# Kernel optimization log

Measured on AMD Instinct MI355X. Metric: run time of the kernel, lower is better.

## Reference

```python
import jax, jax.numpy as jnp
import numpy as np

T = 4.0  # distillation temperature (init kwarg)
B, C = 64, 1000


def _hierarchical_softmax(x, targets):
    # x, targets: [B, C]
    xd = jax.lax.stop_gradient(x)
    # t2[b,i,k] = relu(x[b,i] - stop_grad(x[b,k]))  -> [B, C, C]
    t2 = jnp.maximum(x[:, :, None] - xd[:, None, :], 0.0)
    # t3[b,i] = mean_k targets[b,k] * t2[b,i,k]
    t3 = (targets[:, None, :] * t2).mean(axis=-1)  # [B, C]
    choice = targets * jnp.exp(-t3) + (1.0 - targets)
    ex = jnp.exp(x)
    neg_sum = ((1.0 - targets) * ex).sum(axis=-1, keepdims=True)  # [B, 1]
    return ex / (choice * neg_sum + ex)


def setup_inputs() -> dict:
    key = jax.random.key(0)
    k1, k2, k3 = jax.random.split(key, 3)
    y_s = jax.random.normal(k1, (B, C), dtype=jnp.float32)
    y_t = jax.random.normal(k2, (B, C), dtype=jnp.float32)
    w = jax.random.randint(k3, (B, C), 0, 2).astype(jnp.float32)  # multi-hot targets
    return {"y_s": y_s, "y_t": y_t, "w": w}


def reference(y_s, y_t, w):
    # 'w' branch of DistillKL.forward (dead code: preds/thr/sigmoid/max_min omitted)
    p_s = _hierarchical_softmax(y_s / 4.0, w)
    p_t = _hierarchical_softmax(y_t / 4.0, w)
    p_s_1 = jnp.minimum(p_s, 1.0)  # clamp(max=1)
    p_t_1 = jnp.minimum(p_t, 1.0)
    # abs(...) >= 0 so clamp(min=0,max=1) == min(.,1)
    pos_expo = w * jnp.minimum(jnp.abs((p_t_1 + 1.0) / 2.0 - p_s_1), 1.0) ** 0.25
    neg_expo = (1.0 - w) * jnp.minimum(jnp.abs(p_t_1 / 2.0 - p_s_1), 1.0)
    expt = pos_expo + neg_expo
    ps = jnp.maximum(p_s_1 ** expt, 1e-7)
    pt = jnp.maximum(p_t, 1e-7)
    # my_kl: -(target * log(pred)).sum(dim=1).mean() * T**2
    return -(pt * jnp.log(ps)).sum(axis=1).mean() * (T * T)
```

## Files before the change

kernel.cpp:

```cpp
#include <hip/hip_runtime.h>


#define BN 64
#define CN 1000
#define CPAD 1024
#define SPLITS 8
#define CHUNK 125
#define THREADS 512
#define KQ (CPAD / 4)
#define NEG_LOG_EPS -16.118095650958319f

__global__ __launch_bounds__(THREADS) void distill_part(
    const float* __restrict__ ys, const float* __restrict__ yt,
    const float* __restrict__ w, float* __restrict__ part)
{
    const int b = blockIdx.x;
    const int s = blockIdx.y;
    const int tid = threadIdx.x;
    const int lane = tid & 63;
    const int wid = tid >> 6;
    const int l = tid & 127;
    const int q = tid >> 7;

    __shared__ __align__(16) float xs[CPAD], xt[CPAD];
    __shared__ __align__(16) float xsm[CPAD], xtm[CPAD];
    __shared__ float wsh[CPAD];
    __shared__ float ps_s[THREADS], ps_t[THREADS];
    __shared__ float redns[16];
    __shared__ float redterm[2];

    const float* ysr = ys + b * CN;
    const float* ytr = yt + b * CN;
    const float* wr  = w  + b * CN;

    float ns_s = 0.f, ns_t = 0.f;
    #pragma unroll
    for (int k = tid; k < CPAD; k += THREADS) {
        if (k < CN) {
            float a  = ysr[k] * 0.25f;
            float c2 = ytr[k] * 0.25f;
            float wk = wr[k];
            xs[k] = a; xt[k] = c2; wsh[k] = wk;
            bool pos = (wk != 0.f);
            xsm[k] = pos ? a  : 1e30f;
            xtm[k] = pos ? c2 : 1e30f;
            float nw = 1.f - wk;
            ns_s += nw * expf(a);
            ns_t += nw * expf(c2);
        } else {
            xs[k] = 0.f; xt[k] = 0.f; wsh[k] = 0.f;
            xsm[k] = 1e30f; xtm[k] = 1e30f;
        }
    }
    #pragma unroll
    for (int off = 32; off > 0; off >>= 1) {
        ns_s += __shfl_down(ns_s, off);
        ns_t += __shfl_down(ns_t, off);
    }
    if (lane == 0) { redns[wid * 2] = ns_s; redns[wid * 2 + 1] = ns_t; }
    __syncthreads();
    float negsum_s = 0.f, negsum_t = 0.f;
    #pragma unroll
    for (int u = 0; u < 8; ++u) {
        negsum_s += redns[u * 2];
        negsum_t += redns[u * 2 + 1];
    }

    const int i = s * CHUNK + l;
    const float xsi = xs[i], xti = xt[i];
    const float4* xsm4 = reinterpret_cast<const float4*>(xsm) + q * (KQ / 4);
    const float4* xtm4 = reinterpret_cast<const float4*>(xtm) + q * (KQ / 4);
    float as0 = 0.f, as1 = 0.f, at0 = 0.f, at1 = 0.f;
    #pragma unroll 4
    for (int j = 0; j < KQ / 4; ++j) {
        float4 vs = xsm4[j];
        float4 vt = xtm4[j];
        as0 += fmaxf(xsi - vs.x, 0.f);
        as1 += fmaxf(xsi - vs.y, 0.f);
        as0 += fmaxf(xsi - vs.z, 0.f);
        as1 += fmaxf(xsi - vs.w, 0.f);
        at0 += fmaxf(xti - vt.x, 0.f);
        at1 += fmaxf(xti - vt.y, 0.f);
        at0 += fmaxf(xti - vt.z, 0.f);
        at1 += fmaxf(xti - vt.w, 0.f);
    }
    ps_s[tid] = as0 + as1;
    ps_t[tid] = at0 + at1;
    __syncthreads();

    float term = 0.f;
    if (tid < CHUNK) {
        const float acc_s = ps_s[tid] + ps_s[tid + 128] + ps_s[tid + 256] + ps_s[tid + 384];
        const float acc_t = ps_t[tid] + ps_t[tid + 128] + ps_t[tid + 256] + ps_t[tid + 384];
        const float t3s = acc_s * (1.0f / CN);
        const float t3t = acc_t * (1.0f / CN);
        const float wi = wsh[i];
        const float ch_s = wi * expf(-t3s) + (1.f - wi);
        const float ch_t = wi * expf(-t3t) + (1.f - wi);
        const float exs = expf(xsi), ext = expf(xti);
        const float p_s = exs / (ch_s * negsum_s + exs);
        const float p_t = ext / (ch_t * negsum_t + ext);
        const float ps1 = fminf(p_s, 1.f);
        const float pt1 = fminf(p_t, 1.f);
        const float vpos = fminf(fabsf((pt1 + 1.f) * 0.5f - ps1), 1.f);
        const float vneg = fminf(fabsf(pt1 * 0.5f - ps1), 1.f);
        const float expt = wi * sqrtf(sqrtf(vpos)) + (1.f - wi) * vneg;
        const float logps = fmaxf(expt * logf(ps1), NEG_LOG_EPS);
        term = fmaxf(p_t, 1e-7f) * logps;
    }
    #pragma unroll
    for (int off = 32; off > 0; off >>= 1) term += __shfl_down(term, off);
    if (wid < 2 && lane == 0) redterm[wid] = term;
    __syncthreads();
    if (tid == 0) part[b * SPLITS + s] = redterm[0] + redterm[1];
}

__global__ __launch_bounds__(64) void distill_final(
    const float* __restrict__ part, float* __restrict__ out)
{
    const int t = threadIdx.x;
    float v = 0.f;
    for (int j = t; j < BN * SPLITS; j += 64) v += part[j];
    #pragma unroll
    for (int off = 32; off > 0; off >>= 1) v += __shfl_down(v, off);
    if (t == 0) out[0] = -0.25f * v;
}

extern "C" void kernel_launch(void* const* d_in, const int* in_sizes, int n_in,
                              void* d_out, int out_size, void* d_ws, size_t ws_size,
                              hipStream_t stream) {
    const float* ys = (const float*)d_in[0];
    const float* yt = (const float*)d_in[1];
    const float* w  = (const float*)d_in[2];
    float* out  = (float*)d_out;
    float* part = (float*)d_ws;

    dim3 grid(BN, SPLITS);
    distill_part<<<grid, THREADS, 0, stream>>>(ys, yt, w, part);
    distill_final<<<1, 64, 0, stream>>>(part, out);
}
```

Before: 71.97 us.

## Compact positive-target columns via ballot and register-block two rows per thread

Wavefront 0 stream-compacts the logits whose target is nonzero into contiguous shared arrays using ballot and popcount, padding to a multiple of 32. The pairwise relu sum then runs only over these compacted columns instead of all 1024 padded entries with sentinel values, which roughly halves the inner loop for random multi-hot targets. Each thread also handles two rows against one loaded float4, reusing the LDS loads across both rows. The cost is a serial compaction pass done by a single wavefront, plus an extra barrier before the main loop starts.

```diff
diff --git a/kernel.cpp b/kernel.cpp
--- a/kernel.cpp
+++ b/kernel.cpp
@@ -7,7 +7,6 @@
 #define SPLITS 8
 #define CHUNK 125
 #define THREADS 512
-#define KQ (CPAD / 4)
 #define NEG_LOG_EPS -16.118095650958319f
 
 __global__ __launch_bounds__(THREADS) void distill_part(
@@ -19,15 +18,15 @@
     const int tid = threadIdx.x;
     const int lane = tid & 63;
     const int wid = tid >> 6;
-    const int l = tid & 127;
-    const int q = tid >> 7;
 
     __shared__ __align__(16) float xs[CPAD], xt[CPAD];
-    __shared__ __align__(16) float xsm[CPAD], xtm[CPAD];
+    __shared__ __align__(16) float xsc[CPAD], xtc[CPAD];
     __shared__ float wsh[CPAD];
-    __shared__ float ps_s[THREADS], ps_t[THREADS];
+    __shared__ __align__(16) float ps0s[THREADS], ps1s[THREADS];
+    __shared__ __align__(16) float ps0t[THREADS], ps1t[THREADS];
     __shared__ float redns[16];
     __shared__ float redterm[2];
+    __shared__ int mcnt;
 
     const float* ysr = ys + b * CN;
     const float* ytr = yt + b * CN;
@@ -41,15 +40,11 @@
             float c2 = ytr[k] * 0.25f;
             float wk = wr[k];
             xs[k] = a; xt[k] = c2; wsh[k] = wk;
-            bool pos = (wk != 0.f);
-            xsm[k] = pos ? a  : 1e30f;
-            xtm[k] = pos ? c2 : 1e30f;
             float nw = 1.f - wk;
             ns_s += nw * expf(a);
             ns_t += nw * expf(c2);
         } else {
             xs[k] = 0.f; xt[k] = 0.f; wsh[k] = 0.f;
-            xsm[k] = 1e30f; xtm[k] = 1e30f;
         }
     }
     #pragma unroll
@@ -66,35 +61,67 @@
         negsum_t += redns[u * 2 + 1];
     }
 
-    const int i = s * CHUNK + l;
-    const float xsi = xs[i], xti = xt[i];
-    const float4* xsm4 = reinterpret_cast<const float4*>(xsm) + q * (KQ / 4);
-    const float4* xtm4 = reinterpret_cast<const float4*>(xtm) + q * (KQ / 4);
-    float as0 = 0.f, as1 = 0.f, at0 = 0.f, at1 = 0.f;
-    #pragma unroll 4
-    for (int j = 0; j < KQ / 4; ++j) {
-        float4 vs = xsm4[j];
-        float4 vt = xtm4[j];
-        as0 += fmaxf(xsi - vs.x, 0.f);
-        as1 += fmaxf(xsi - vs.y, 0.f);
-        as0 += fmaxf(xsi - vs.z, 0.f);
-        as1 += fmaxf(xsi - vs.w, 0.f);
-        at0 += fmaxf(xti - vt.x, 0.f);
-        at1 += fmaxf(xti - vt.y, 0.f);
-        at0 += fmaxf(xti - vt.z, 0.f);
-        at1 += fmaxf(xti - vt.w, 0.f);
+    if (wid == 0) {
+        int base = 0;
+        for (int k0 = 0; k0 < CPAD; k0 += 64) {
+            const int k = k0 + lane;
+            const bool pos = (wsh[k] != 0.f);
+            const unsigned long long mask = __ballot(pos);
+            const int pre = __popcll(mask & ((1ull << lane) - 1ull));
+            if (pos) { xsc[base + pre] = xs[k]; xtc[base + pre] = xt[k]; }
+            base += __popcll(mask);
+        }
+        const int mp = (base + 31) & ~31;
+        for (int m = base + lane; m < mp; m += 64) { xsc[m] = 1e30f; xtc[m] = 1e30f; }
+        if (lane == 0) mcnt = mp;
     }
-    ps_s[tid] = as0 + as1;
-    ps_t[tid] = at0 + at1;
+    __syncthreads();
+
+    const int Mpad = mcnt;
+    const int SL4  = Mpad >> 5;
+    const int il = tid & 63;
+    const int q  = tid >> 6;
+    const int i0 = s * CHUNK + il;
+    const bool has2 = (il < CHUNK - 64);
+    const int i1 = has2 ? i0 + 64 : i0;
+    const float xsi0 = xs[i0], xti0 = xt[i0];
+    const float xsi1 = xs[i1], xti1 = xt[i1];
+    const float4* s4 = reinterpret_cast<const float4*>(xsc) + q * SL4;
+    const float4* t4 = reinterpret_cast<const float4*>(xtc) + q * SL4;
+    float a0s = 0.f, a1s = 0.f, a0t = 0.f, a1t = 0.f;
+    #pragma unroll 2
+    for (int j = 0; j < SL4; ++j) {
+        const float4 vs = s4[j];
+        const float4 vt = t4[j];
+        a0s += (fmaxf(xsi0 - vs.x, 0.f) + fmaxf(xsi0 - vs.y, 0.f))
+             + (fmaxf(xsi0 - vs.z, 0.f) + fmaxf(xsi0 - vs.w, 0.f));
+        a1s += (fmaxf(xsi1 - vs.x, 0.f) + fmaxf(xsi1 - vs.y, 0.f))
+             + (fmaxf(xsi1 - vs.z, 0.f) + fmaxf(xsi1 - vs.w, 0.f));
+        a0t += (fmaxf(xti0 - vt.x, 0.f) + fmaxf(xti0 - vt.y, 0.f))
+             + (fmaxf(xti0 - vt.z, 0.f) + fmaxf(xti0 - vt.w, 0.f));
+        a1t += (fmaxf(xti1 - vt.x, 0.f) + fmaxf(xti1 - vt.y, 0.f))
+             + (fmaxf(xti1 - vt.z, 0.f) + fmaxf(xti1 - vt.w, 0.f));
+    }
+    ps0s[tid] = a0s; ps1s[tid] = a1s;
+    ps0t[tid] = a0t; ps1t[tid] = a1t;
     __syncthreads();
 
     float term = 0.f;
     if (tid < CHUNK) {
-        const float acc_s = ps_s[tid] + ps_s[tid + 128] + ps_s[tid + 256] + ps_s[tid + 384];
-        const float acc_t = ps_t[tid] + ps_t[tid + 128] + ps_t[tid + 256] + ps_t[tid + 384];
+        const int i = s * CHUNK + tid;
+        const float* bs = (tid < 64) ? ps0s : ps1s;
+        const float* bt = (tid < 64) ? ps0t : ps1t;
+        const int off = tid & 63;
+        float acc_s = 0.f, acc_t = 0.f;
+        #pragma unroll
+        for (int qq = 0; qq < 8; ++qq) {
+            acc_s += bs[qq * 64 + off];
+            acc_t += bt[qq * 64 + off];
+        }
         const float t3s = acc_s * (1.0f / CN);
         const float t3t = acc_t * (1.0f / CN);
         const float wi = wsh[i];
+        const float xsi = xs[i], xti = xt[i];
         const float ch_s = wi * expf(-t3s) + (1.f - wi);
         const float ch_t = wi * expf(-t3t) + (1.f - wi);
         const float exs = expf(xsi), ext = expf(xti);
```

Result: faster. 68.45 us (-4.9%).
